# Optimization experiments

Hardware: AMD Instinct MI355X
Metric: run time of the kernel (lower is better)

## Reference

```python
import jax, jax.numpy as jnp
import numpy as np

B = 64          # graphs per batch
NPG = 4000      # nodes per graph
CPG0 = 400      # level-0 clusters per graph
CPG1 = 40       # level-1 clusters per graph
DEG = 8         # avg degree
F_IN = 64       # node feature dim (input_shape)


def setup_inputs() -> dict:
    rng = np.random.RandomState(0)
    N0 = B * NPG
    E0 = N0 * DEG
    N1 = B * CPG0
    N2 = B * CPG1
    # node -> graph and node -> level-0 cluster (globally consecutive ids)
    node_graph = np.repeat(np.arange(N0 // NPG), NPG)
    local = np.tile(np.arange(NPG), B)
    cluster0 = node_graph * CPG0 + local // (NPG // CPG0)
    # random edges, endpoints within the same graph
    edge_graph = np.repeat(np.arange(B), NPG * DEG)
    src = edge_graph * NPG + rng.randint(0, NPG, size=E0)
    dst = edge_graph * NPG + rng.randint(0, NPG, size=E0)
    edge_index = np.stack([src, dst]).astype(np.int64)
    # community_pooling's pool_edge: map edges through cluster0, drop self-loops,
    # coalesce duplicates (edge_attr summed). Precompute the integer structure.
    ci, cj = cluster0[src], cluster0[dst]
    mask = ci != cj
    key_ = ci.astype(np.int64) * N1 + cj.astype(np.int64)
    uniq, inv = np.unique(key_[mask], return_inverse=True)
    E1 = uniq.shape[0]
    edge_seg = np.full(E0, E1, dtype=np.int64)   # dropped self-loops -> dummy seg E1
    edge_seg[mask] = inv
    edge_index1 = np.stack([uniq // N1, uniq % N1]).astype(np.int64)
    # level-1 clusters on pooled nodes and graph id of each level-1 cluster
    cl_idx = np.arange(N1)
    cluster1 = (cl_idx // CPG0) * CPG1 + (cl_idx % CPG0) // (CPG0 // CPG1)
    batch2 = np.arange(N2) // CPG1

    key = jax.random.key(0)
    ks = jax.random.split(key, 10)

    def lin(k, fin, fout):
        return jax.random.normal(k, (fin, fout), jnp.float32) / np.sqrt(fin)

    return dict(
        x=jax.random.normal(ks[0], (N0, F_IN), jnp.float32),
        edge_attr=jax.random.uniform(ks[1], (E0, 1), jnp.float32),
        edge_index=jnp.asarray(edge_index),
        cluster0=jnp.asarray(cluster0.astype(np.int64)),
        edge_index1=jnp.asarray(edge_index1),
        edge_seg=jnp.asarray(edge_seg),
        cluster1=jnp.asarray(cluster1.astype(np.int64)),
        batch2=jnp.asarray(batch2.astype(np.int64)),
        n_clusters0=N1, n_clusters1=N2, n_graphs=B,
        W1=lin(ks[2], F_IN, 16), We1=lin(ks[3], 1, 1), Wa1=lin(ks[4], 2 * 16 + 1, 1),
        W2=lin(ks[5], 16, 32), We2=lin(ks[6], 1, 1), Wa2=lin(ks[7], 2 * 32 + 1, 1),
        fc1_W=lin(ks[8], 32, 64), fc1_b=jnp.zeros((64,), jnp.float32),
        fc2_W=lin(ks[9], 64, 1), fc2_b=jnp.zeros((1,), jnp.float32),
    )


def _gin_conv(x, edge_index, edge_attr, W, We, Wa, num_nodes):
    # DeepRank-GNN GINetConvLayer (all linears bias-free)
    row, col = edge_index[0], edge_index[1]
    xp = x @ W                      # project once, then gather (same math as fc(x[col]))
    xrow, xcol = xp[row], xp[col]   # (E, out)
    ed = edge_attr @ We             # (E, n_edge_feat)
    alpha = jnp.concatenate([xrow, xcol, ed], axis=1) @ Wa   # (E, 1)
    alpha = jax.nn.leaky_relu(alpha)
    # faithful: softmax over dim=1 of an (E,1) tensor -> all ones
    alpha = jax.nn.softmax(alpha, axis=1)
    h = alpha * xcol
    return jax.ops.segment_sum(h, row, num_segments=num_nodes)


def reference(x, edge_attr, edge_index, cluster0, edge_index1, edge_seg,
              cluster1, batch2, n_clusters0, n_clusters1, n_graphs,
              W1, We1, Wa1, W2, We2, Wa2, fc1_W, fc1_b, fc2_W, fc2_b):
    # conv1 + relu
    x1 = jax.nn.relu(_gin_conv(x, edge_index, edge_attr, W1, We1, Wa1, x.shape[0]))
    # community_pooling: scatter_max nodes onto clusters, coalesced pooled edges
    x_pool = jax.ops.segment_max(x1, cluster0, num_segments=n_clusters0)
    E1 = edge_index1.shape[1]
    ea1 = jax.ops.segment_sum(edge_attr, edge_seg, num_segments=E1 + 1)[:E1]
    # conv2 + relu on pooled graph
    x2 = jax.nn.relu(_gin_conv(x_pool, edge_index1, ea1, W2, We2, Wa2, n_clusters0))
    # max_pool_x over level-1 clusters, then scatter_mean per graph
    x3 = jax.ops.segment_max(x2, cluster1, num_segments=n_clusters1)
    s = jax.ops.segment_sum(x3, batch2, num_segments=n_graphs)
    cnt = jax.ops.segment_sum(jnp.ones((x3.shape[0], 1), x3.dtype), batch2,
                              num_segments=n_graphs)
    xg = s / cnt                                  # (B, 32)
    h = jax.nn.relu(xg @ fc1_W + fc1_b)           # (B, 64)
    return h @ fc2_W + fc2_b                      # (B, 1)
```

## Files before the change

### kernel.cpp

```cpp
#include <hip/hip_runtime.h>


#define C1 16
#define C2 32
#define NPG 4000
#define EPG 32000
#define NPQ 1000
#define ELLW 32
#define SCW 34

__global__ __launch_bounds__(256) void pre_k(const float* __restrict__ x,
                                             const float* __restrict__ W,
                                             float* __restrict__ xp1) {
    __shared__ float xs[64][65];
    __shared__ float Ws[64][16];
    int t = threadIdx.x;
    int n0 = blockIdx.x * 64;
    const float4* xg = (const float4*)(x + (size_t)n0 * 64);
    for (int i = t; i < 1024; i += 256) {
        float4 v = xg[i];
        int r = i >> 4, c4 = (i & 15) * 4;
        xs[r][c4] = v.x; xs[r][c4 + 1] = v.y;
        xs[r][c4 + 2] = v.z; xs[r][c4 + 3] = v.w;
    }
    {
        float4 wv = ((const float4*)W)[t];
        int r = t >> 2, c4 = (t & 3) * 4;
        Ws[r][c4] = wv.x; Ws[r][c4 + 1] = wv.y;
        Ws[r][c4 + 2] = wv.z; Ws[r][c4 + 3] = wv.w;
    }
    __syncthreads();
    int r = t >> 2, q = t & 3;
    float4 acc = make_float4(0.f, 0.f, 0.f, 0.f);
#pragma unroll
    for (int k = 0; k < 64; ++k) {
        float xv = xs[r][k];
        acc.x += xv * Ws[k][q * 4 + 0];
        acc.y += xv * Ws[k][q * 4 + 1];
        acc.z += xv * Ws[k][q * 4 + 2];
        acc.w += xv * Ws[k][q * 4 + 3];
    }
    ((float4*)xp1)[(size_t)(n0 + r) * 4 + q] = acc;
}

__global__ __launch_bounds__(1024) void sortagg_k(const int* __restrict__ ei,
                                                  const float* __restrict__ xp1,
                                                  float* __restrict__ xpool,
                                                  const int* __restrict__ ei1,
                                                  int* __restrict__ rp1,
                                                  int E0, int E1, int N1,
                                                  int B, int cpg) {
    __shared__ int cnt[NPQ];
    __shared__ unsigned short sc16[NPQ * SCW];
    int bid = blockIdx.x;
    int t = threadIdx.x;
    if (bid >= 256) {
        int e = (bid - 256) * 1024 + t;
        if (e >= E1) return;
        int r = ei1[e];
        int rprev = __shfl_up(r, 1);
        if ((t & 63) == 0) rprev = (e == 0) ? -1 : ei1[e - 1];
        for (int rr = rprev + 1; rr <= r; ++rr) rp1[rr] = e;
        if (e == E1 - 1)
            for (int rr = r + 1; rr <= N1; ++rr) rp1[rr] = E1;
        return;
    }
    int g = bid % B;
    int q = bid / B;
    const int4* rows4 = (const int4*)(ei + (size_t)g * EPG);
    const int4* cols4 = (const int4*)(ei + E0 + (size_t)g * EPG);
    int gbase = g * NPG;
    int rbase = gbase + q * NPQ;

    for (int i = t; i < NPQ; i += 1024) cnt[i] = 0;
    __syncthreads();
    for (int i = t; i < EPG / 4; i += 1024) {
        int4 r4 = rows4[i];
        int4 c4 = cols4[i];
        int rl, pos;
        rl = r4.x - rbase;
        if ((unsigned)rl < NPQ) {
            pos = atomicAdd(&cnt[rl], 1);
            if (pos < ELLW) sc16[rl * SCW + pos] = (unsigned short)(c4.x - gbase);
        }
        rl = r4.y - rbase;
        if ((unsigned)rl < NPQ) {
            pos = atomicAdd(&cnt[rl], 1);
            if (pos < ELLW) sc16[rl * SCW + pos] = (unsigned short)(c4.y - gbase);
        }
        rl = r4.z - rbase;
        if ((unsigned)rl < NPQ) {
            pos = atomicAdd(&cnt[rl], 1);
            if (pos < ELLW) sc16[rl * SCW + pos] = (unsigned short)(c4.z - gbase);
        }
        rl = r4.w - rbase;
        if ((unsigned)rl < NPQ) {
            pos = atomicAdd(&cnt[rl], 1);
            if (pos < ELLW) sc16[rl * SCW + pos] = (unsigned short)(c4.w - gbase);
        }
    }
    __syncthreads();
    if (t < 800) {
        int cl = t >> 3, f4 = (t >> 1) & 3, h = t & 1;
        const float4* xp = (const float4*)xp1 + (size_t)gbase * 4;
        float4 m = make_float4(-1e30f, -1e30f, -1e30f, -1e30f);
#pragma unroll
        for (int j = 0; j < 5; ++j) {
            int r = cl * 10 + h * 5 + j;
            int cn = cnt[r];
            const unsigned short* er = &sc16[r * SCW];
            float4 s = make_float4(0.f, 0.f, 0.f, 0.f);
#pragma unroll
            for (int k = 0; k < 16; ++k) {
                if (k < cn) {
                    float4 v = xp[(size_t)er[k] * 4 + f4];
                    s.x += v.x; s.y += v.y; s.z += v.z; s.w += v.w;
                }
            }
            for (int k = 16; k < cn; ++k) {
                float4 v = xp[(size_t)er[k] * 4 + f4];
                s.x += v.x; s.y += v.y; s.z += v.z; s.w += v.w;
            }
            m.x = fmaxf(m.x, s.x); m.y = fmaxf(m.y, s.y);
            m.z = fmaxf(m.z, s.z); m.w = fmaxf(m.w, s.w);
        }
        m.x = fmaxf(m.x, __shfl_xor(m.x, 1));
        m.y = fmaxf(m.y, __shfl_xor(m.y, 1));
        m.z = fmaxf(m.z, __shfl_xor(m.z, 1));
        m.w = fmaxf(m.w, __shfl_xor(m.w, 1));
        if (h == 0) {
            m.x = fmaxf(m.x, 0.f); m.y = fmaxf(m.y, 0.f);
            m.z = fmaxf(m.z, 0.f); m.w = fmaxf(m.w, 0.f);
            ((float4*)xpool)[(size_t)(g * cpg + q * 100 + cl) * 4 + f4] = m;
        }
    }
}

__global__ __launch_bounds__(256) void agg2v2_k(const int* __restrict__ ei1,
                                                const int* __restrict__ rp,
                                                const float* __restrict__ xpool,
                                                const float* __restrict__ W2,
                                                float* __restrict__ x3,
                                                int E1, int B, int cpg) {
    __shared__ float sums[20][C1];
    __shared__ float x2s[20][C2];
    int g = blockIdx.x % B;
    int c = blockIdx.x / B;
    int t = threadIdx.x;
    int lane = t & 63, w = t >> 6;
    int f4 = lane & 3, es = lane >> 2;
    const int* col = ei1 + E1;
    for (int j = w; j < 20; j += 4) {
        int r = g * cpg + c * 20 + j;
        int e0 = rp[r], e1e = rp[r + 1];
        float4 acc = make_float4(0.f, 0.f, 0.f, 0.f);
#pragma unroll
        for (int k = 0; k < 8; ++k) {
            int e = e0 + es + 16 * k;
            if (e < e1e) {
                float4 v = ((const float4*)(xpool + (size_t)col[e] * C1))[f4];
                acc.x += v.x; acc.y += v.y; acc.z += v.z; acc.w += v.w;
            }
        }
        for (int e = e0 + es + 128; e < e1e; e += 16) {
            float4 v = ((const float4*)(xpool + (size_t)col[e] * C1))[f4];
            acc.x += v.x; acc.y += v.y; acc.z += v.z; acc.w += v.w;
        }
#pragma unroll
        for (int off = 4; off <= 32; off <<= 1) {
            acc.x += __shfl_xor(acc.x, off);
            acc.y += __shfl_xor(acc.y, off);
            acc.z += __shfl_xor(acc.z, off);
            acc.w += __shfl_xor(acc.w, off);
        }
        if (es == 0) {
            sums[j][f4 * 4 + 0] = acc.x;
            sums[j][f4 * 4 + 1] = acc.y;
            sums[j][f4 * 4 + 2] = acc.z;
            sums[j][f4 * 4 + 3] = acc.w;
        }
    }
    __syncthreads();
    for (int i = t; i < 20 * C2; i += 256) {
        int rl = i >> 5, jf = i & 31;
        float v = 0.f;
#pragma unroll
        for (int k = 0; k < C1; ++k) v += sums[rl][k] * W2[k * C2 + jf];
        x2s[rl][jf] = v;
    }
    __syncthreads();
    if (t < 64) {
        int cl = t >> 5, f = t & 31;
        float m = x2s[cl * 10][f];
#pragma unroll
        for (int k = 1; k < 10; ++k) m = fmaxf(m, x2s[cl * 10 + k][f]);
        x3[((size_t)g * 40 + c * 2 + cl) * C2 + f] = fmaxf(m, 0.f);
    }
}

__global__ __launch_bounds__(64) void head_k(const float* __restrict__ x3,
                                             const float* __restrict__ fc1W,
                                             const float* __restrict__ fc1b,
                                             const float* __restrict__ fc2W,
                                             const float* __restrict__ fc2b,
                                             float* __restrict__ out) {
    __shared__ float xgs[C2];
    int g = blockIdx.x;
    int t = threadIdx.x;
    if (t < C2) {
        const float* base = x3 + (size_t)g * 40 * C2 + t;
        float s = 0.f;
#pragma unroll
        for (int cl = 0; cl < 40; ++cl) s += base[cl * C2];
        xgs[t] = s;
    }
    __syncthreads();
    float h = fc1b[t];
#pragma unroll
    for (int f = 0; f < C2; ++f) h += xgs[f] * (1.f / 40.f) * fc1W[f * 64 + t];
    h = fmaxf(h, 0.f);
    float v = h * fc2W[t];
#pragma unroll
    for (int off = 32; off > 0; off >>= 1) v += __shfl_down(v, off);
    if (t == 0) out[g] = v + fc2b[0];
}

extern "C" void kernel_launch(void* const* d_in, const int* in_sizes, int n_in,
                              void* d_out, int out_size, void* d_ws, size_t ws_size,
                              hipStream_t stream) {
    const float* x    = (const float*)d_in[0];
    const int*   ei   = (const int*)d_in[2];
    const int*   ei1  = (const int*)d_in[4];
    const float* W1   = (const float*)d_in[11];
    const float* W2   = (const float*)d_in[14];
    const float* fc1W = (const float*)d_in[17];
    const float* fc1b = (const float*)d_in[18];
    const float* fc2W = (const float*)d_in[19];
    const float* fc2b = (const float*)d_in[20];
    float* out = (float*)d_out;

    const int N0 = in_sizes[0] / 64;
    const int E0 = in_sizes[2] / 2;
    const int E1 = in_sizes[4] / 2;
    const int N1 = in_sizes[6];
    const int N2 = in_sizes[7];
    const int B  = N2 / 40;
    const int CPG0 = N1 / B;

    float* xp1   = (float*)d_ws;
    float* xpool = xp1 + (size_t)N0 * C1;
    float* x3    = xpool + (size_t)N1 * C1;
    int*   rp1   = (int*)(x3 + (size_t)B * 40 * C2);

    const int RB = (E1 + 1023) / 1024;

    pre_k<<<N0 / 64, 256, 0, stream>>>(x, W1, xp1);
    sortagg_k<<<256 + RB, 1024, 0, stream>>>(ei, xp1, xpool, ei1, rp1,
                                             E0, E1, N1, B, CPG0);
    agg2v2_k<<<B * (CPG0 / 20), 256, 0, stream>>>(ei1, rp1, xpool, W2, x3,
                                                  E1, B, CPG0);
    head_k<<<B, 64, 0, stream>>>(x3, fc1W, fc1b, fc2W, fc2b, out);
}
```

Measured before the change: 214.9 us.

## Fuse first-layer projection into sortagg kernel and batch row-pointer construction

Removes the separate pre_k launch. Each sortagg block now computes the x·W1 projection for its whole graph in 256-row shared-memory chunks before building its ELL adjacency. The row-pointer blocks also handle RPK edges per thread, so fewer blocks are launched. The cost is that all four quarter-blocks of a graph recompute and rewrite the full projection, reading x four times. The extra shared-memory tile also raises LDS use per block, which limits occupancy.

```diff
diff --git a/kernel.cpp b/kernel.cpp
--- a/kernel.cpp
+++ b/kernel.cpp
@@ -8,43 +8,12 @@
 #define NPQ 1000
 #define ELLW 32
 #define SCW 34
-
-__global__ __launch_bounds__(256) void pre_k(const float* __restrict__ x,
-                                             const float* __restrict__ W,
-                                             float* __restrict__ xp1) {
-    __shared__ float xs[64][65];
-    __shared__ float Ws[64][16];
-    int t = threadIdx.x;
-    int n0 = blockIdx.x * 64;
-    const float4* xg = (const float4*)(x + (size_t)n0 * 64);
-    for (int i = t; i < 1024; i += 256) {
-        float4 v = xg[i];
-        int r = i >> 4, c4 = (i & 15) * 4;
-        xs[r][c4] = v.x; xs[r][c4 + 1] = v.y;
-        xs[r][c4 + 2] = v.z; xs[r][c4 + 3] = v.w;
-    }
-    {
-        float4 wv = ((const float4*)W)[t];
-        int r = t >> 2, c4 = (t & 3) * 4;
-        Ws[r][c4] = wv.x; Ws[r][c4 + 1] = wv.y;
-        Ws[r][c4 + 2] = wv.z; Ws[r][c4 + 3] = wv.w;
-    }
-    __syncthreads();
-    int r = t >> 2, q = t & 3;
-    float4 acc = make_float4(0.f, 0.f, 0.f, 0.f);
-#pragma unroll
-    for (int k = 0; k < 64; ++k) {
-        float xv = xs[r][k];
-        acc.x += xv * Ws[k][q * 4 + 0];
-        acc.y += xv * Ws[k][q * 4 + 1];
-        acc.z += xv * Ws[k][q * 4 + 2];
-        acc.w += xv * Ws[k][q * 4 + 3];
-    }
-    ((float4*)xp1)[(size_t)(n0 + r) * 4 + q] = acc;
-}
-
-__global__ __launch_bounds__(1024) void sortagg_k(const int* __restrict__ ei,
-                                                  const float* __restrict__ xp1,
+#define RPK 8
+
+__global__ __launch_bounds__(1024) void sortagg_k(const float* __restrict__ x,
+                                                  const float* __restrict__ W1,
+                                                  float* __restrict__ xp1,
+                                                  const int* __restrict__ ei,
                                                   float* __restrict__ xpool,
                                                   const int* __restrict__ ei1,
                                                   int* __restrict__ rp1,
@@ -52,28 +21,70 @@
                                                   int B, int cpg) {
     __shared__ int cnt[NPQ];
     __shared__ unsigned short sc16[NPQ * SCW];
+    __shared__ float xs[256][65];
+    __shared__ float Ws[64][16];
     int bid = blockIdx.x;
     int t = threadIdx.x;
     if (bid >= 256) {
-        int e = (bid - 256) * 1024 + t;
-        if (e >= E1) return;
-        int r = ei1[e];
-        int rprev = __shfl_up(r, 1);
-        if ((t & 63) == 0) rprev = (e == 0) ? -1 : ei1[e - 1];
-        for (int rr = rprev + 1; rr <= r; ++rr) rp1[rr] = e;
-        if (e == E1 - 1)
-            for (int rr = r + 1; rr <= N1; ++rr) rp1[rr] = E1;
+        int base = (bid - 256) * (1024 * RPK);
+        for (int ii = 0; ii < RPK; ++ii) {
+            int e = base + ii * 1024 + t;
+            if (e < E1) {
+                int r = ei1[e];
+                int rprev = __shfl_up(r, 1);
+                if ((t & 63) == 0) rprev = (e == 0) ? -1 : ei1[e - 1];
+                for (int rr = rprev + 1; rr <= r; ++rr) rp1[rr] = e;
+                if (e == E1 - 1)
+                    for (int rr = r + 1; rr <= N1; ++rr) rp1[rr] = E1;
+            }
+        }
         return;
     }
     int g = bid % B;
     int q = bid / B;
+    int gbase = g * NPG;
+    int rbase = gbase + q * NPQ;
+
+    for (int i = t; i < NPQ; i += 1024) cnt[i] = 0;
+    if (t < 256) {
+        float4 wv = ((const float4*)W1)[t];
+        int r = t >> 2, c4 = (t & 3) * 4;
+        Ws[r][c4] = wv.x; Ws[r][c4 + 1] = wv.y;
+        Ws[r][c4 + 2] = wv.z; Ws[r][c4 + 3] = wv.w;
+    }
+    __syncthreads();
+    const float* xg = x + (size_t)gbase * 64;
+    float4* xp1g = (float4*)xp1 + (size_t)gbase * 4;
+    for (int i = 0; i < 16; ++i) {
+        int cc = (q * 4 + i) & 15;
+        int r0 = cc * 256;
+        int nr = (NPG - r0 < 256) ? (NPG - r0) : 256;
+        const float4* xc = (const float4*)(xg + (size_t)r0 * 64);
+        for (int j = t; j < nr * 16; j += 1024) {
+            float4 v = xc[j];
+            int r = j >> 4, c4 = (j & 15) * 4;
+            xs[r][c4] = v.x; xs[r][c4 + 1] = v.y;
+            xs[r][c4 + 2] = v.z; xs[r][c4 + 3] = v.w;
+        }
+        __syncthreads();
+        int r = t >> 2, q4 = t & 3;
+        if (r < nr) {
+            float4 acc = make_float4(0.f, 0.f, 0.f, 0.f);
+#pragma unroll
+            for (int k = 0; k < 64; ++k) {
+                float xv = xs[r][k];
+                acc.x += xv * Ws[k][q4 * 4 + 0];
+                acc.y += xv * Ws[k][q4 * 4 + 1];
+                acc.z += xv * Ws[k][q4 * 4 + 2];
+                acc.w += xv * Ws[k][q4 * 4 + 3];
+            }
+            xp1g[(size_t)(r0 + r) * 4 + q4] = acc;
+        }
+        __syncthreads();
+    }
+
     const int4* rows4 = (const int4*)(ei + (size_t)g * EPG);
     const int4* cols4 = (const int4*)(ei + E0 + (size_t)g * EPG);
-    int gbase = g * NPG;
-    int rbase = gbase + q * NPQ;
-
-    for (int i = t; i < NPQ; i += 1024) cnt[i] = 0;
-    __syncthreads();
     for (int i = t; i < EPG / 4; i += 1024) {
         int4 r4 = rows4[i];
         int4 c4 = cols4[i];
@@ -100,6 +111,7 @@
         }
     }
     __syncthreads();
+
     if (t < 800) {
         int cl = t >> 3, f4 = (t >> 1) & 3, h = t & 1;
         const float4* xp = (const float4*)xp1 + (size_t)gbase * 4;
@@ -252,10 +264,9 @@
     float* x3    = xpool + (size_t)N1 * C1;
     int*   rp1   = (int*)(x3 + (size_t)B * 40 * C2);
 
-    const int RB = (E1 + 1023) / 1024;
-
-    pre_k<<<N0 / 64, 256, 0, stream>>>(x, W1, xp1);
-    sortagg_k<<<256 + RB, 1024, 0, stream>>>(ei, xp1, xpool, ei1, rp1,
+    const int RB = (E1 + 1024 * RPK - 1) / (1024 * RPK);
+
+    sortagg_k<<<256 + RB, 1024, 0, stream>>>(x, W1, xp1, ei, xpool, ei1, rp1,
                                              E0, E1, N1, B, CPG0);
     agg2v2_k<<<B * (CPG0 / 20), 256, 0, stream>>>(ei1, rp1, xpool, W2, x3,
                                                   E1, B, CPG0);
```

Measured after the change: 273.5 us. +27.3%, slower.
